# Performance work log

Measured on AMD Instinct MI355X. Metric: run time of the kernel, lower is better.

Reference implementation:

```python
import jax, jax.numpy as jnp
import numpy as np

D_MODEL, D_K, D_V, HEAD = 512, 512, 512, 8
SCALE = 1.0 / np.sqrt(D_K)  # torch code divides by sqrt(d_k) (full d_k, not head_dim)
NEG = -1.0e9


def setup_inputs() -> dict:
    key = jax.random.key(0)
    ks = jax.random.split(key, 10)
    B, S = 2, 4096
    x = jax.random.normal(ks[0], (B, S, D_MODEL), dtype=jnp.float32)
    mask = jax.random.randint(ks[1], (B, S), 0, 2, dtype=jnp.int32)
    s = 1.0 / np.sqrt(D_MODEL)
    Wq = jax.random.normal(ks[2], (D_MODEL, D_K), dtype=jnp.float32) * s
    bq = jnp.zeros((D_K,), jnp.float32)
    Wk = jax.random.normal(ks[3], (D_MODEL, D_K), dtype=jnp.float32) * s
    bk = jnp.zeros((D_K,), jnp.float32)
    Wv = jax.random.normal(ks[4], (D_MODEL, D_V), dtype=jnp.float32) * s
    bv = jnp.zeros((D_V,), jnp.float32)
    Wo = jax.random.normal(ks[5], (D_V, D_MODEL), dtype=jnp.float32) * s
    bo = jnp.zeros((D_MODEL,), jnp.float32)
    return {"x": x, "mask": mask, "Wq": Wq, "bq": bq, "Wk": Wk, "bk": bk,
            "Wv": Wv, "bv": bv, "Wo": Wo, "bo": bo}


def reference(x, mask, Wq, bq, Wk, bk, Wv, bv, Wo, bo):
    B, S, _ = x.shape
    hd_k = D_K // HEAD
    hd_v = D_V // HEAD
    # projections -> [B, H, S, hd]
    Q = (x @ Wq + bq).reshape(B, S, HEAD, hd_k).transpose(0, 2, 1, 3)
    K = (x @ Wk + bk).reshape(B, S, HEAD, hd_k).transpose(0, 2, 1, 3)
    V = (x @ Wv + bv).reshape(B, S, HEAD, hd_v).transpose(0, 2, 1, 3)
    # scores [B, H, S, S], scaled by 1/sqrt(d_k) (full d_k, faithful to source)
    scores = jnp.einsum('bhqd,bhkd->bhqk', Q, K) * SCALE
    m = (mask == 1)[:, None, None, :]  # [B,1,1,S]
    scores = jnp.where(m, NEG, scores)
    attn = jax.nn.softmax(scores, axis=-1)
    out = jnp.einsum('bhqk,bhkd->bhqd', attn, V)  # [B,H,S,hd_v]
    out = out.transpose(0, 2, 1, 3).reshape(B, S, D_V)
    return out @ Wo + bo
```

## Files before the change

### kernel.cpp

```cpp
#include <hip/hip_runtime.h>
#include <hip/hip_bf16.h>
#include <stdint.h>

typedef __attribute__((ext_vector_type(8))) short bf16x8;
typedef __attribute__((ext_vector_type(4))) float f32x4;
typedef __attribute__((ext_vector_type(16))) float f32x16;
typedef __attribute__((ext_vector_type(4))) unsigned int u32x4;

#define MFMA16(a, b, c) __builtin_amdgcn_mfma_f32_16x16x32_bf16(a, b, c, 0, 0, 0)
#define MFMA32(a, b, c) __builtin_amdgcn_mfma_f32_32x32x16_bf16(a, b, c, 0, 0, 0)

constexpr float QSCALE = 0.04419417382415922f * 1.4426950408889634f;

__device__ __forceinline__ void gload_lds16(const void* g, void* l) {
  __builtin_amdgcn_global_load_lds((const __attribute__((address_space(1))) uint32_t*)g,
                                   (__attribute__((address_space(3))) uint32_t*)l, 16, 0, 0);
}
__device__ __forceinline__ bf16x8 lds_read_swz(const short* base, int row, int ch) {
  return *(const bf16x8*)((const char*)base + row * 128 + (((ch ^ row) & 7) << 4));
}
__device__ __forceinline__ short f2b(float f) {
  __hip_bfloat16 h = __float2bfloat16(f);
  return *reinterpret_cast<short*>(&h);
}
__device__ __forceinline__ float exp2fast(float x) {
#if __has_builtin(__builtin_amdgcn_exp2f)
  return __builtin_amdgcn_exp2f(x);
#else
  return exp2f(x);
#endif
}

__global__ void k_cvt_x(const float* __restrict__ x, short* __restrict__ xb) {
  const int i = blockIdx.x * 256 + threadIdx.x;
  const float4 v = ((const float4*)x)[i];
  short4 o;
  o.x = f2b(v.x); o.y = f2b(v.y); o.z = f2b(v.z); o.w = f2b(v.w);
  ((short4*)xb)[i] = o;
}

__global__ void k_cvt_w(const float* __restrict__ wq, const float* __restrict__ wk,
                        const float* __restrict__ wv, const float* __restrict__ wo,
                        short* __restrict__ wt) {
  const int gid = blockIdx.x * 256 + threadIdx.x;
  const int mat = gid >> 18;
  const int idx = gid & 262143;
  const int n = idx >> 9, k = idx & 511;
  const float* w = (mat == 0) ? wq : (mat == 1) ? wk : (mat == 2) ? wv : wo;
  wt[gid] = f2b(w[k * 512 + n]);
}

__global__ void k_scan(const int* __restrict__ mask, int* __restrict__ perm,
                       int* __restrict__ cnt) {
  __shared__ int ws[16];
  const int b = blockIdx.x, tid = threadIdx.x;
  const int lane = tid & 63, w = tid >> 6;
  const int* m = mask + b * 4096;
  int v[4], s = 0;
#pragma unroll
  for (int j = 0; j < 4; ++j) { v[j] = (m[tid * 4 + j] == 0) ? 1 : 0; s += v[j]; }
  int sc = s;
  for (int d = 1; d < 64; d <<= 1) { int t = __shfl_up(sc, d); if (lane >= d) sc += t; }
  if (lane == 63) ws[w] = sc;
  __syncthreads();
  if (tid == 0) {
    int acc = 0;
    for (int i = 0; i < 16; ++i) { int t = ws[i]; ws[i] = acc; acc += t; }
    cnt[b] = acc;
  }
  __syncthreads();
  int pos = ws[w] + sc - s;
  int* p = perm + b * 4096;
#pragma unroll
  for (int j = 0; j < 4; ++j) { p[tid * 4 + j] = v[j] ? pos : -1; pos += v[j]; }
}

template <int MODE>
__global__ __launch_bounds__(256, 2) void k_gemm2(
    const short* __restrict__ A, const short* __restrict__ W,
    const float* __restrict__ bq, const float* __restrict__ bk,
    const float* __restrict__ bv, const int* __restrict__ perm,
    short* __restrict__ oq, short* __restrict__ ok, short* __restrict__ ov,
    float* __restrict__ fo) {
  __shared__ short Asm[2][128 * 64];
  __shared__ short Bsm[2][128 * 64];
  const int tid = threadIdx.x;
  const int wave = tid >> 6, lane = tid & 63;
  const int lane15 = lane & 15, g = lane >> 4;
  const int wm = wave >> 1, wn = wave & 1;
  const int m0 = blockIdx.x * 128;
  const int n0 = blockIdx.y * 128;

  const char* Ag = (const char*)A + (size_t)m0 * 1024;
  const char* Bg = (const char*)W + (size_t)n0 * 1024;

  f32x4 acc[4][4] = {};

  auto stage = [&](int buf, int kt) {
    const int k0b = kt * 128;
#pragma unroll
    for (int q = 0; q < 4; ++q) {
      int s_ = (wave * 4 + q) * 64 + lane;
      int row = s_ >> 3, ch = s_ & 7;
      gload_lds16(Ag + (size_t)row * 1024 + k0b + (((ch ^ row) & 7) << 4),
                  (char*)&Asm[buf][0] + s_ * 16);
      gload_lds16(Bg + (size_t)row * 1024 + k0b + (((ch ^ row) & 7) << 4),
                  (char*)&Bsm[buf][0] + s_ * 16);
    }
  };

  stage(0, 0);
  asm volatile("s_waitcnt vmcnt(0)" ::: "memory");
  __syncthreads();

  for (int kt = 0; kt < 8; ++kt) {
    const int cur = kt & 1;
    if (kt < 7) stage(cur ^ 1, kt + 1);
#pragma unroll
    for (int kk = 0; kk < 2; ++kk) {
      bf16x8 af[4], bfr[4];
#pragma unroll
      for (int m = 0; m < 4; ++m)
        af[m] = lds_read_swz(&Asm[cur][0], wm * 64 + m * 16 + lane15, kk * 4 + g);
#pragma unroll
      for (int n = 0; n < 4; ++n)
        bfr[n] = lds_read_swz(&Bsm[cur][0], wn * 64 + n * 16 + lane15, kk * 4 + g);
      __builtin_amdgcn_s_setprio(1);
#pragma unroll
      for (int m = 0; m < 4; ++m)
#pragma unroll
        for (int n = 0; n < 4; ++n)
          acc[m][n] = MFMA16(af[m], bfr[n], acc[m][n]);
      __builtin_amdgcn_s_setprio(0);
    }
    asm volatile("s_waitcnt vmcnt(0)" ::: "memory");
    __syncthreads();
  }

#pragma unroll
  for (int nf = 0; nf < 4; ++nf) {
    const int col = n0 + wn * 64 + nf * 16 + lane15;
    if constexpr (MODE == 0) {
      const int mat = col >> 9, nn = col & 511;
      const int hh = nn >> 6, d = nn & 63;
      const float bias = ((mat == 0) ? bq : (mat == 1) ? bk : bv)[nn];
      const int dk = d >> 4, hb = (d >> 3) & 1, jj = d & 7;
#pragma unroll
      for (int mf = 0; mf < 4; ++mf) {
#pragma unroll
        for (int j = 0; j < 4; ++j) {
          const int rowg = m0 + wm * 64 + mf * 16 + g * 4 + j;
          const int b_ = rowg >> 12, sl = rowg & 4095;
          const size_t bh = (size_t)(b_ * 8 + hh);
          const float v = acc[mf][nf][j] + bias;
          if (mat == 0) {
            oq[bh * 262144 +
               (size_t)(((sl >> 5) * 4 + dk) * 64 + hb * 32 + (sl & 31)) * 8 + jj] =
                f2b(v * QSCALE);
          } else {
            const int pm_ = perm[b_ * 4096 + sl];
            if (pm_ >= 0) {
              const int t = pm_ >> 6, r = pm_ & 63;
              if (mat == 1) {
                ok[bh * 262144 +
                   (size_t)((t * 8 + dk * 2 + (r >> 5)) * 64 + hb * 32 + (r & 31)) * 8 + jj] =
                    f2b(v);
              } else {
                const int mm = (r & ~12) | (((r >> 2) & 1) << 3) | (((r >> 3) & 1) << 2);
                ov[bh * 262144 +
                   (size_t)((t * 8 + ((mm >> 4) & 3) * 2 + (d >> 5)) * 64 +
                            ((mm >> 3) & 1) * 32 + (d & 31)) * 8 + (mm & 7)] = f2b(v);
              }
            }
          }
        }
      }
    } else {
      const float bias = bq[col];
#pragma unroll
      for (int mf = 0; mf < 4; ++mf)
#pragma unroll
        for (int j = 0; j < 4; ++j) {
          const int rowg = m0 + wm * 64 + mf * 16 + g * 4 + j;
          fo[(size_t)rowg * 512 + col] = acc[mf][nf][j] + bias;
        }
    }
  }
}

#define ATT_BODY(T, KC, KN)                                                   \
  {                                                                           \
    bf16x8 v0_ = vld(T, 0), v1_ = vld(T, 1), v2_ = vld(T, 2), v3_ = vld(T, 3),\
           v4_ = vld(T, 4), v5_ = vld(T, 5), v6_ = vld(T, 6), v7_ = vld(T, 7);\
    f32x16 s0v = {}, s1v = {};                                                \
    __builtin_amdgcn_s_setprio(1);                                            \
    _Pragma("unroll") for (int dk = 0; dk < 4; ++dk) {                        \
      s0v = MFMA32(KC[2 * dk], qreg[dk], s0v);                                \
      s1v = MFMA32(KC[2 * dk + 1], qreg[dk], s1v);                            \
    }                                                                         \
    __builtin_amdgcn_s_setprio(0);                                            \
    _Pragma("unroll") for (int u = 0; u < 8; ++u) KN[u] = kld((T) + 1, u);    \
    if ((T) == nt - 1 && lim < 64) {                                          \
      _Pragma("unroll") for (int i = 0; i < 16; ++i) {                        \
        const int r0 = (i & 3) + 8 * (i >> 2) + 4 * h;                        \
        if (r0 >= lim) s0v[i] = -1e30f;                                       \
        if (r0 + 32 >= lim) s1v[i] = -1e30f;                                  \
      }                                                                       \
    }                                                                         \
    unsigned int wA[8], wB[8];                                                \
    float ts = 0.f;                                                           \
    _Pragma("unroll") for (int j2 = 0; j2 < 8; ++j2) {                        \
      float a0 = exp2fast(s0v[2 * j2]);                                       \
      float a1 = exp2fast(s0v[2 * j2 + 1]);                                   \
      float b0 = exp2fast(s1v[2 * j2]);                                       \
      float b1 = exp2fast(s1v[2 * j2 + 1]);                                   \
      ts += (a0 + a1) + (b0 + b1);                                            \
      asm("v_cvt_pk_bf16_f32 %0, %1, %2" : "=v"(wA[j2]) : "v"(a0), "v"(a1));  \
      asm("v_cvt_pk_bf16_f32 %0, %1, %2" : "=v"(wB[j2]) : "v"(b0), "v"(b1));  \
    }                                                                         \
    l_ += ts;                                                                 \
    __builtin_amdgcn_s_setprio(1);                                            \
    {                                                                         \
      union PU { u32x4 u; bf16x8 f; } pu;                                     \
      pu.u[0] = wA[0]; pu.u[1] = wA[1]; pu.u[2] = wA[2]; pu.u[3] = wA[3];     \
      o0 = MFMA32(v0_, pu.f, o0); o1 = MFMA32(v1_, pu.f, o1);                 \
      pu.u[0] = wA[4]; pu.u[1] = wA[5]; pu.u[2] = wA[6]; pu.u[3] = wA[7];     \
      o0 = MFMA32(v2_, pu.f, o0); o1 = MFMA32(v3_, pu.f, o1);                 \
      pu.u[0] = wB[0]; pu.u[1] = wB[1]; pu.u[2] = wB[2]; pu.u[3] = wB[3];     \
      o0 = MFMA32(v4_, pu.f, o0); o1 = MFMA32(v5_, pu.f, o1);                 \
      pu.u[0] = wB[4]; pu.u[1] = wB[5]; pu.u[2] = wB[6]; pu.u[3] = wB[7];     \
      o0 = MFMA32(v6_, pu.f, o0); o1 = MFMA32(v7_, pu.f, o1);                 \
    }                                                                         \
    __builtin_amdgcn_s_setprio(0);                                            \
  }

__global__ __launch_bounds__(256, 2) void k_attn(
    const short* __restrict__ Qp, const short* __restrict__ Kp,
    const short* __restrict__ Vp, const int* __restrict__ cnt,
    short* __restrict__ out) {
  const int tid = threadIdx.x;
  const int wave = tid >> 6, lane = tid & 63;
  const int l31 = lane & 31, h = lane >> 5;
  const int bh = blockIdx.y, b = bh >> 3, hh = bh & 7;
  const int qb = blockIdx.x * 4 + wave;

  const short* Qg = Qp + (size_t)bh * 262144;
  const short* Kg = Kp + (size_t)bh * 262144;
  const short* Vg = Vp + (size_t)bh * 262144;

  auto kld = [&](int t, int u) {
    return *(const bf16x8*)(Kg + ((size_t)(t * 8 + u) * 64 + lane) * 8);
  };
  auto vld = [&](int t, int u) {
    return *(const bf16x8*)(Vg + ((size_t)(t * 8 + u) * 64 + lane) * 8);
  };

  bf16x8 qreg[4];
#pragma unroll
  for (int dk = 0; dk < 4; ++dk)
    qreg[dk] = *(const bf16x8*)(Qg + ((size_t)(qb * 4 + dk) * 64 + lane) * 8);

  const int cn = cnt[b];
  const int nt = max(1, (cn + 63) >> 6);
  const int lim = cn - (nt - 1) * 64;

  bf16x8 ka[8], kb[8];
#pragma unroll
  for (int u = 0; u < 8; ++u) ka[u] = kld(0, u);

  f32x16 o0 = {}, o1 = {};
  float l_ = 0.f;

  for (int t = 0; t < nt; t += 2) {
    ATT_BODY(t, ka, kb);
    if (t + 1 < nt) ATT_BODY(t + 1, kb, ka);
  }

  l_ += __shfl_xor(l_, 32);
  const float inv = 1.0f / l_;
  short* og = out + (size_t)(b * 4096 + qb * 32 + l31) * 512 + hh * 64;
#pragma unroll
  for (int r2 = 0; r2 < 4; ++r2) {
    {
      const int base = 8 * r2 + 4 * h;
      short4 s4;
      s4.x = f2b(o0[4 * r2 + 0] * inv);
      s4.y = f2b(o0[4 * r2 + 1] * inv);
      s4.z = f2b(o0[4 * r2 + 2] * inv);
      s4.w = f2b(o0[4 * r2 + 3] * inv);
      *(short4*)(og + base) = s4;
    }
    {
      const int base = 32 + 8 * r2 + 4 * h;
      short4 s4;
      s4.x = f2b(o1[4 * r2 + 0] * inv);
      s4.y = f2b(o1[4 * r2 + 1] * inv);
      s4.z = f2b(o1[4 * r2 + 2] * inv);
      s4.w = f2b(o1[4 * r2 + 3] * inv);
      *(short4*)(og + base) = s4;
    }
  }
}

extern "C" void kernel_launch(void* const* d_in, const int* in_sizes, int n_in,
                              void* d_out, int out_size, void* d_ws, size_t ws_size,
                              hipStream_t stream) {
  const float* x  = (const float*)d_in[0];
  const int* mask = (const int*)d_in[1];
  const float* Wq = (const float*)d_in[2];
  const float* bq = (const float*)d_in[3];
  const float* Wk = (const float*)d_in[4];
  const float* bk = (const float*)d_in[5];
  const float* Wv = (const float*)d_in[6];
  const float* bv = (const float*)d_in[7];
  const float* Wo = (const float*)d_in[8];
  const float* bo = (const float*)d_in[9];
  float* out = (float*)d_out;

  short* xb   = (short*)d_ws;
  short* wt   = xb + (size_t)8192 * 512;
  short* qws  = wt + (size_t)4 * 512 * 512;
  short* kws  = qws + (size_t)8192 * 512;
  short* vws  = kws + (size_t)8192 * 512;
  short* aout = vws + (size_t)8192 * 512;
  int* perm   = (int*)(aout + (size_t)8192 * 512);
  int* cntw   = perm + 8192;

  k_cvt_x<<<4096, 256, 0, stream>>>(x, xb);
  k_cvt_w<<<4096, 256, 0, stream>>>(Wq, Wk, Wv, Wo, wt);
  k_scan<<<2, 1024, 0, stream>>>(mask, perm, cntw);
  k_gemm2<0><<<dim3(64, 12), 256, 0, stream>>>(xb, wt, bq, bk, bv, perm,
                                               qws, kws, vws, nullptr);
  k_attn<<<dim3(32, 16), 256, 0, stream>>>(qws, kws, vws, cntw, aout);
  k_gemm2<1><<<dim3(64, 4), 256, 0, stream>>>(aout, wt + (size_t)3 * 512 * 512, bo,
                                              nullptr, nullptr, nullptr,
                                              nullptr, nullptr, nullptr, out);
}
```

Measured before the change: 184.8 us.

## Stage attention K/V tiles through LDS and split output GEMM into narrower tiles

The attention kernel now loads each K/V tile once per block into double-buffered shared memory with async global-to-LDS loads. Previously each of the four waves read K and V directly from global memory into registers. The block index is remapped so consecutive blocks spread across heads and query tiles. The output projection becomes its own kernel with 128x64 tiles, doubling the grid for better CU occupancy. The cost is a block-wide barrier per KV tile, plus LDS read latency in the inner loop.

```diff
diff --git a/kernel.cpp b/kernel.cpp
--- a/kernel.cpp
+++ b/kernel.cpp
@@ -75,13 +75,11 @@
   for (int j = 0; j < 4; ++j) { p[tid * 4 + j] = v[j] ? pos : -1; pos += v[j]; }
 }
 
-template <int MODE>
-__global__ __launch_bounds__(256, 2) void k_gemm2(
+__global__ __launch_bounds__(256, 2) void k_gemmqkv(
     const short* __restrict__ A, const short* __restrict__ W,
     const float* __restrict__ bq, const float* __restrict__ bk,
     const float* __restrict__ bv, const int* __restrict__ perm,
-    short* __restrict__ oq, short* __restrict__ ok, short* __restrict__ ov,
-    float* __restrict__ fo) {
+    short* __restrict__ oq, short* __restrict__ ok, short* __restrict__ ov) {
   __shared__ short Asm[2][128 * 64];
   __shared__ short Bsm[2][128 * 64];
   const int tid = threadIdx.x;
@@ -140,121 +138,140 @@
 #pragma unroll
   for (int nf = 0; nf < 4; ++nf) {
     const int col = n0 + wn * 64 + nf * 16 + lane15;
-    if constexpr (MODE == 0) {
-      const int mat = col >> 9, nn = col & 511;
-      const int hh = nn >> 6, d = nn & 63;
-      const float bias = ((mat == 0) ? bq : (mat == 1) ? bk : bv)[nn];
-      const int dk = d >> 4, hb = (d >> 3) & 1, jj = d & 7;
-#pragma unroll
-      for (int mf = 0; mf < 4; ++mf) {
-#pragma unroll
-        for (int j = 0; j < 4; ++j) {
-          const int rowg = m0 + wm * 64 + mf * 16 + g * 4 + j;
-          const int b_ = rowg >> 12, sl = rowg & 4095;
-          const size_t bh = (size_t)(b_ * 8 + hh);
-          const float v = acc[mf][nf][j] + bias;
-          if (mat == 0) {
-            oq[bh * 262144 +
-               (size_t)(((sl >> 5) * 4 + dk) * 64 + hb * 32 + (sl & 31)) * 8 + jj] =
-                f2b(v * QSCALE);
-          } else {
-            const int pm_ = perm[b_ * 4096 + sl];
-            if (pm_ >= 0) {
-              const int t = pm_ >> 6, r = pm_ & 63;
-              if (mat == 1) {
-                ok[bh * 262144 +
-                   (size_t)((t * 8 + dk * 2 + (r >> 5)) * 64 + hb * 32 + (r & 31)) * 8 + jj] =
-                    f2b(v);
-              } else {
-                const int mm = (r & ~12) | (((r >> 2) & 1) << 3) | (((r >> 3) & 1) << 2);
-                ov[bh * 262144 +
-                   (size_t)((t * 8 + ((mm >> 4) & 3) * 2 + (d >> 5)) * 64 +
-                            ((mm >> 3) & 1) * 32 + (d & 31)) * 8 + (mm & 7)] = f2b(v);
-              }
+    const int mat = col >> 9, nn = col & 511;
+    const int hh = nn >> 6, d = nn & 63;
+    const float bias = ((mat == 0) ? bq : (mat == 1) ? bk : bv)[nn];
+    const int dk = d >> 4, hb = (d >> 3) & 1, jj = d & 7;
+#pragma unroll
+    for (int mf = 0; mf < 4; ++mf) {
+#pragma unroll
+      for (int j = 0; j < 4; ++j) {
+        const int rowg = m0 + wm * 64 + mf * 16 + g * 4 + j;
+        const int b_ = rowg >> 12, sl = rowg & 4095;
+        const size_t bh = (size_t)(b_ * 8 + hh);
+        const float v = acc[mf][nf][j] + bias;
+        if (mat == 0) {
+          oq[bh * 262144 +
+             (size_t)(((sl >> 5) * 4 + dk) * 64 + hb * 32 + (sl & 31)) * 8 + jj] =
+              f2b(v * QSCALE);
+        } else {
+          const int pm_ = perm[b_ * 4096 + sl];
+          if (pm_ >= 0) {
+            const int t = pm_ >> 6, r = pm_ & 63;
+            if (mat == 1) {
+              ok[bh * 262144 +
+                 (size_t)((t * 8 + dk * 2 + (r >> 5)) * 64 + hb * 32 + (r & 31)) * 8 + jj] =
+                  f2b(v);
+            } else {
+              const int mm = (r & ~12) | (((r >> 2) & 1) << 3) | (((r >> 3) & 1) << 2);
+              ov[bh * 262144 +
+                 (size_t)((t * 8 + ((mm >> 4) & 3) * 2 + (d >> 5)) * 64 +
+                          ((mm >> 3) & 1) * 32 + (d & 31)) * 8 + (mm & 7)] = f2b(v);
             }
           }
         }
       }
-    } else {
-      const float bias = bq[col];
-#pragma unroll
-      for (int mf = 0; mf < 4; ++mf)
-#pragma unroll
-        for (int j = 0; j < 4; ++j) {
-          const int rowg = m0 + wm * 64 + mf * 16 + g * 4 + j;
-          fo[(size_t)rowg * 512 + col] = acc[mf][nf][j] + bias;
-        }
-    }
-  }
-}
-
-#define ATT_BODY(T, KC, KN)                                                   \
-  {                                                                           \
-    bf16x8 v0_ = vld(T, 0), v1_ = vld(T, 1), v2_ = vld(T, 2), v3_ = vld(T, 3),\
-           v4_ = vld(T, 4), v5_ = vld(T, 5), v6_ = vld(T, 6), v7_ = vld(T, 7);\
-    f32x16 s0v = {}, s1v = {};                                                \
-    __builtin_amdgcn_s_setprio(1);                                            \
-    _Pragma("unroll") for (int dk = 0; dk < 4; ++dk) {                        \
-      s0v = MFMA32(KC[2 * dk], qreg[dk], s0v);                                \
-      s1v = MFMA32(KC[2 * dk + 1], qreg[dk], s1v);                            \
-    }                                                                         \
-    __builtin_amdgcn_s_setprio(0);                                            \
-    _Pragma("unroll") for (int u = 0; u < 8; ++u) KN[u] = kld((T) + 1, u);    \
-    if ((T) == nt - 1 && lim < 64) {                                          \
-      _Pragma("unroll") for (int i = 0; i < 16; ++i) {                        \
-        const int r0 = (i & 3) + 8 * (i >> 2) + 4 * h;                        \
-        if (r0 >= lim) s0v[i] = -1e30f;                                       \
-        if (r0 + 32 >= lim) s1v[i] = -1e30f;                                  \
-      }                                                                       \
-    }                                                                         \
-    unsigned int wA[8], wB[8];                                                \
-    float ts = 0.f;                                                           \
-    _Pragma("unroll") for (int j2 = 0; j2 < 8; ++j2) {                        \
-      float a0 = exp2fast(s0v[2 * j2]);                                       \
-      float a1 = exp2fast(s0v[2 * j2 + 1]);                                   \
-      float b0 = exp2fast(s1v[2 * j2]);                                       \
-      float b1 = exp2fast(s1v[2 * j2 + 1]);                                   \
-      ts += (a0 + a1) + (b0 + b1);                                            \
-      asm("v_cvt_pk_bf16_f32 %0, %1, %2" : "=v"(wA[j2]) : "v"(a0), "v"(a1));  \
-      asm("v_cvt_pk_bf16_f32 %0, %1, %2" : "=v"(wB[j2]) : "v"(b0), "v"(b1));  \
-    }                                                                         \
-    l_ += ts;                                                                 \
-    __builtin_amdgcn_s_setprio(1);                                            \
-    {                                                                         \
-      union PU { u32x4 u; bf16x8 f; } pu;                                     \
-      pu.u[0] = wA[0]; pu.u[1] = wA[1]; pu.u[2] = wA[2]; pu.u[3] = wA[3];     \
-      o0 = MFMA32(v0_, pu.f, o0); o1 = MFMA32(v1_, pu.f, o1);                 \
-      pu.u[0] = wA[4]; pu.u[1] = wA[5]; pu.u[2] = wA[6]; pu.u[3] = wA[7];     \
-      o0 = MFMA32(v2_, pu.f, o0); o1 = MFMA32(v3_, pu.f, o1);                 \
-      pu.u[0] = wB[0]; pu.u[1] = wB[1]; pu.u[2] = wB[2]; pu.u[3] = wB[3];     \
-      o0 = MFMA32(v4_, pu.f, o0); o1 = MFMA32(v5_, pu.f, o1);                 \
-      pu.u[0] = wB[4]; pu.u[1] = wB[5]; pu.u[2] = wB[6]; pu.u[3] = wB[7];     \
-      o0 = MFMA32(v6_, pu.f, o0); o1 = MFMA32(v7_, pu.f, o1);                 \
-    }                                                                         \
-    __builtin_amdgcn_s_setprio(0);                                            \
-  }
+    }
+  }
+}
+
+__global__ __launch_bounds__(256, 2) void k_gemmo(
+    const short* __restrict__ A, const short* __restrict__ W,
+    const float* __restrict__ bias, float* __restrict__ fo) {
+  __shared__ short Asm[2][128 * 64];
+  __shared__ short Bsm[2][64 * 64];
+  const int tid = threadIdx.x;
+  const int wave = tid >> 6, lane = tid & 63;
+  const int lane15 = lane & 15, g = lane >> 4;
+  const int wm = wave >> 1, wn = wave & 1;
+  const int m0 = blockIdx.x * 128;
+  const int n0 = blockIdx.y * 64;
+
+  const char* Ag = (const char*)A + (size_t)m0 * 1024;
+  const char* Bg = (const char*)W + (size_t)n0 * 1024;
+
+  f32x4 acc[4][2] = {};
+
+  auto stage = [&](int buf, int kt) {
+    const int k0b = kt * 128;
+#pragma unroll
+    for (int q = 0; q < 4; ++q) {
+      int s_ = (wave * 4 + q) * 64 + lane;
+      int row = s_ >> 3, ch = s_ & 7;
+      gload_lds16(Ag + (size_t)row * 1024 + k0b + (((ch ^ row) & 7) << 4),
+                  (char*)&Asm[buf][0] + s_ * 16);
+    }
+#pragma unroll
+    for (int q = 0; q < 2; ++q) {
+      int s_ = (wave * 2 + q) * 64 + lane;
+      int row = s_ >> 3, ch = s_ & 7;
+      gload_lds16(Bg + (size_t)row * 1024 + k0b + (((ch ^ row) & 7) << 4),
+                  (char*)&Bsm[buf][0] + s_ * 16);
+    }
+  };
+
+  stage(0, 0);
+  asm volatile("s_waitcnt vmcnt(0)" ::: "memory");
+  __syncthreads();
+
+  for (int kt = 0; kt < 8; ++kt) {
+    const int cur = kt & 1;
+    if (kt < 7) stage(cur ^ 1, kt + 1);
+#pragma unroll
+    for (int kk = 0; kk < 2; ++kk) {
+      bf16x8 af[4], bfr[2];
+#pragma unroll
+      for (int m = 0; m < 4; ++m)
+        af[m] = lds_read_swz(&Asm[cur][0], wm * 64 + m * 16 + lane15, kk * 4 + g);
+#pragma unroll
+      for (int n = 0; n < 2; ++n)
+        bfr[n] = lds_read_swz(&Bsm[cur][0], wn * 32 + n * 16 + lane15, kk * 4 + g);
+      __builtin_amdgcn_s_setprio(1);
+#pragma unroll
+      for (int m = 0; m < 4; ++m)
+#pragma unroll
+        for (int n = 0; n < 2; ++n)
+          acc[m][n] = MFMA16(af[m], bfr[n], acc[m][n]);
+      __builtin_amdgcn_s_setprio(0);
+    }
+    asm volatile("s_waitcnt vmcnt(0)" ::: "memory");
+    __syncthreads();
+  }
+
+#pragma unroll
+  for (int nf = 0; nf < 2; ++nf) {
+    const int col = n0 + wn * 32 + nf * 16 + lane15;
+    const float b = bias[col];
+#pragma unroll
+    for (int mf = 0; mf < 4; ++mf)
+#pragma unroll
+      for (int j = 0; j < 4; ++j) {
+        const int rowg = m0 + wm * 64 + mf * 16 + g * 4 + j;
+        fo[(size_t)rowg * 512 + col] = acc[mf][nf][j] + b;
+      }
+  }
+}
 
 __global__ __launch_bounds__(256, 2) void k_attn(
     const short* __restrict__ Qp, const short* __restrict__ Kp,
     const short* __restrict__ Vp, const int* __restrict__ cnt,
     short* __restrict__ out) {
+  __shared__ short Ks[2][8][512];
+  __shared__ short Vs[2][8][512];
+
   const int tid = threadIdx.x;
   const int wave = tid >> 6, lane = tid & 63;
   const int l31 = lane & 31, h = lane >> 5;
-  const int bh = blockIdx.y, b = bh >> 3, hh = bh & 7;
-  const int qb = blockIdx.x * 4 + wave;
+  const int bid = blockIdx.x;
+  const int sid = (bid & 7) * 64 + (bid >> 3);
+  const int qt = sid & 31, bh = sid >> 5;
+  const int b = bh >> 3, hh = bh & 7;
+  const int qb = qt * 4 + wave;
 
   const short* Qg = Qp + (size_t)bh * 262144;
   const short* Kg = Kp + (size_t)bh * 262144;
   const short* Vg = Vp + (size_t)bh * 262144;
 
-  auto kld = [&](int t, int u) {
-    return *(const bf16x8*)(Kg + ((size_t)(t * 8 + u) * 64 + lane) * 8);
-  };
-  auto vld = [&](int t, int u) {
-    return *(const bf16x8*)(Vg + ((size_t)(t * 8 + u) * 64 + lane) * 8);
-  };
-
   bf16x8 qreg[4];
 #pragma unroll
   for (int dk = 0; dk < 4; ++dk)
@@ -264,16 +281,76 @@
   const int nt = max(1, (cn + 63) >> 6);
   const int lim = cn - (nt - 1) * 64;
 
-  bf16x8 ka[8], kb[8];
-#pragma unroll
-  for (int u = 0; u < 8; ++u) ka[u] = kld(0, u);
+  auto stage = [&](int buf, int t) {
+#pragma unroll
+    for (int q = 0; q < 2; ++q) {
+      const int u = wave * 2 + q;
+      gload_lds16(Kg + ((size_t)(t * 8 + u) * 64 + lane) * 8, &Ks[buf][u][lane * 8]);
+      gload_lds16(Vg + ((size_t)(t * 8 + u) * 64 + lane) * 8, &Vs[buf][u][lane * 8]);
+    }
+  };
+  auto ldsK = [&](int buf, int u) { return *(const bf16x8*)&Ks[buf][u][lane * 8]; };
+  auto ldsV = [&](int buf, int u) { return *(const bf16x8*)&Vs[buf][u][lane * 8]; };
 
   f32x16 o0 = {}, o1 = {};
   float l_ = 0.f;
 
-  for (int t = 0; t < nt; t += 2) {
-    ATT_BODY(t, ka, kb);
-    if (t + 1 < nt) ATT_BODY(t + 1, kb, ka);
+  stage(0, 0);
+  __syncthreads();
+
+  for (int t = 0; t < nt; ++t) {
+    const int cur = t & 1;
+    if (t + 1 < nt) stage(cur ^ 1, t + 1);
+
+    f32x16 s0v = {}, s1v = {};
+    __builtin_amdgcn_s_setprio(1);
+#pragma unroll
+    for (int dk = 0; dk < 4; ++dk) {
+      s0v = MFMA32(ldsK(cur, 2 * dk), qreg[dk], s0v);
+      s1v = MFMA32(ldsK(cur, 2 * dk + 1), qreg[dk], s1v);
+    }
+    __builtin_amdgcn_s_setprio(0);
+
+    if (t == nt - 1 && lim < 64) {
+#pragma unroll
+      for (int i = 0; i < 16; ++i) {
+        const int r0 = (i & 3) + 8 * (i >> 2) + 4 * h;
+        if (r0 >= lim) s0v[i] = -1e30f;
+        if (r0 + 32 >= lim) s1v[i] = -1e30f;
+      }
+    }
+
+    unsigned int wA[8], wB[8];
+    float ts = 0.f;
+#pragma unroll
+    for (int j2 = 0; j2 < 8; ++j2) {
+      float a0 = exp2fast(s0v[2 * j2]);
+      float a1 = exp2fast(s0v[2 * j2 + 1]);
+      float b0 = exp2fast(s1v[2 * j2]);
+      float b1 = exp2fast(s1v[2 * j2 + 1]);
+      ts += (a0 + a1) + (b0 + b1);
+      asm("v_cvt_pk_bf16_f32 %0, %1, %2" : "=v"(wA[j2]) : "v"(a0), "v"(a1));
+      asm("v_cvt_pk_bf16_f32 %0, %1, %2" : "=v"(wB[j2]) : "v"(b0), "v"(b1));
+    }
+    l_ += ts;
+
+    __builtin_amdgcn_s_setprio(1);
+#pragma unroll
+    for (int s = 0; s < 4; ++s) {
+      const bf16x8 v0 = ldsV(cur, 2 * s);
+      const bf16x8 v1 = ldsV(cur, 2 * s + 1);
+      const unsigned int* w = (s < 2) ? wA : wB;
+      union PU { u32x4 u; bf16x8 f; } pu;
+      pu.u[0] = w[4 * (s & 1) + 0];
+      pu.u[1] = w[4 * (s & 1) + 1];
+      pu.u[2] = w[4 * (s & 1) + 2];
+      pu.u[3] = w[4 * (s & 1) + 3];
+      o0 = MFMA32(v0, pu.f, o0);
+      o1 = MFMA32(v1, pu.f, o1);
+    }
+    __builtin_amdgcn_s_setprio(0);
+
+    __syncthreads();
   }
 
   l_ += __shfl_xor(l_, 32);
@@ -329,10 +406,7 @@
   k_cvt_x<<<4096, 256, 0, stream>>>(x, xb);
   k_cvt_w<<<4096, 256, 0, stream>>>(Wq, Wk, Wv, Wo, wt);
   k_scan<<<2, 1024, 0, stream>>>(mask, perm, cntw);
-  k_gemm2<0><<<dim3(64, 12), 256, 0, stream>>>(xb, wt, bq, bk, bv, perm,
-                                               qws, kws, vws, nullptr);
-  k_attn<<<dim3(32, 16), 256, 0, stream>>>(qws, kws, vws, cntw, aout);
-  k_gemm2<1><<<dim3(64, 4), 256, 0, stream>>>(aout, wt + (size_t)3 * 512 * 512, bo,
-                                              nullptr, nullptr, nullptr,
-                                              nullptr, nullptr, nullptr, out);
-}
+  k_gemmqkv<<<dim3(64, 12), 256, 0, stream>>>(xb, wt, bq, bk, bv, perm, qws, kws, vws);
+  k_attn<<<512, 256, 0, stream>>>(qws, kws, vws, cntw, aout);
+  k_gemmo<<<dim3(64, 8), 256, 0, stream>>>(aout, wt + (size_t)3 * 512 * 512, bo, out);
+}
```

Result: faster. 180.4 us (-2.3%).
